# Kernel optimization log

Measured on AMD Instinct MI355X. Metric: run time of the kernel, lower is better.

The kernel has to match this reference:

```python
import jax, jax.numpy as jnp
import numpy as np

N, S, I, L, M = 4096, 8, 256, 512, 256


def setup_inputs() -> dict:
    key = jax.random.key(0)
    ks = jax.random.split(key, 13)
    sc_in = 1.0 / np.sqrt(I + L)
    sc_out = 1.0 / np.sqrt(L)
    return {
        "modulation": jax.random.normal(ks[0], (N, S * I), jnp.float32),
        "h0": jax.random.normal(ks[1], (N, S * L), jnp.float32),
        "c0": jax.random.normal(ks[2], (N, S * L), jnp.float32),
        "Wi": jax.random.normal(ks[3], (S, L, I + L), jnp.float32) * sc_in,
        "bi": jnp.full((S, L), -1.0, jnp.float32),  # init_input bias
        "Wf": jax.random.normal(ks[4], (S, L, I + L), jnp.float32) * sc_in,
        "bf": jnp.full((S, L), 1.0, jnp.float32),   # init_forget bias
        "Wg": jax.random.normal(ks[5], (S, L, I + L), jnp.float32) * sc_in,
        "bg": jnp.zeros((S, L), jnp.float32),
        "Wo": jax.random.normal(ks[6], (S, L, I + L), jnp.float32) * sc_in,
        "bo": jnp.zeros((S, L), jnp.float32),
        "Wy": jax.random.normal(ks[7], (S, M, L), jnp.float32) * sc_out,
        "by": jnp.zeros((S, M), jnp.float32),
    }


def reference(modulation, h0, c0, Wi, bi, Wf, bf, Wg, bg, Wo, bo, Wy, by):
    n = modulation.shape[0]
    x = modulation.reshape(n, S, I)          # [N,S,I]
    h = h0.reshape(n, S, L)                  # [N,S,L]
    c = c0.reshape(n, S, L)
    xh = jnp.concatenate([x, h], axis=-1)    # cat_groups: per-stream [x_s, h_s] -> [N,S,I+L]
    # grouped per-stream linear projections for the four gates
    i = jax.nn.sigmoid(jnp.einsum('nsd,sld->nsl', xh, Wi) + bi)
    f = jax.nn.sigmoid(jnp.einsum('nsd,sld->nsl', xh, Wf) + bf)
    g = jnp.tanh(jnp.einsum('nsd,sld->nsl', xh, Wg) + bg)
    o = jax.nn.sigmoid(jnp.einsum('nsd,sld->nsl', xh, Wo) + bo)
    c_new = f * c + i * g
    h_new = o * jnp.tanh(c_new)              # dropout p=0 -> identity
    y = jnp.einsum('nsl,sml->nsm', h_new, Wy) + by
    return y.reshape(n, S * M)
```

## Files before the change

### kernel.cpp

```cpp
#include <hip/hip_runtime.h>
#include <stdint.h>

#define S_ 8
#define N_ 4096
#define I_ 256
#define L_ 512
#define M_ 256
#define D_ 768

typedef __bf16 bf16x8 __attribute__((ext_vector_type(8)));
typedef float f32x4 __attribute__((ext_vector_type(4)));
typedef unsigned short ushort_t;

__device__ __forceinline__ unsigned short f2bf(float f) {
  union { float f; uint32_t u; } c; c.f = f;
  uint32_t u = c.u;
  uint32_t r = u + 0x7FFFu + ((u >> 16) & 1u);
  return (unsigned short)(r >> 16);
}

__device__ __forceinline__ float fsigmoid(float x) {
  return 1.0f / (1.0f + __expf(-x));
}
__device__ __forceinline__ float ftanh(float x) {
  float ax = fabsf(x);
  float e = __expf(-2.0f * ax);
  float t = (1.0f - e) / (1.0f + e);
  return copysignf(t, x);
}

#define GLD16(gsrc, ldst)                                                                  \
  __builtin_amdgcn_global_load_lds(                                                        \
      (const __attribute__((address_space(1))) uint32_t*)(uintptr_t)(gsrc),                \
      (__attribute__((address_space(3))) uint32_t*)(uintptr_t)(ldst), 16, 0, 0)


__global__ __launch_bounds__(256) void cast_bf16_kernel(const float* __restrict__ src,
                                                        ushort_t* __restrict__ dst, int n4) {
  int t = blockIdx.x * 256 + threadIdx.x;
  int stride = gridDim.x * 256;
  for (; t < n4; t += stride) {
    float4 v = ((const float4*)src)[t];
    ushort4 o;
    o.x = f2bf(v.x); o.y = f2bf(v.y); o.z = f2bf(v.z); o.w = f2bf(v.w);
    ((ushort4*)dst)[t] = o;
  }
}

__global__ __launch_bounds__(256) void build_xh_kernel(const float* __restrict__ mod,
                                                       const float* __restrict__ h0,
                                                       ushort_t* __restrict__ xh) {
  int t = blockIdx.x * 256 + threadIdx.x;
  const int total = S_ * N_ * (D_ / 4);
  int stride = gridDim.x * 256;
  for (; t < total; t += stride) {
    int row = t / (D_ / 4);
    int c = t - row * (D_ / 4);
    int s = row >> 12;
    int n = row & (N_ - 1);
    float4 v;
    if (c < I_ / 4)
      v = *(const float4*)(mod + (size_t)n * (S_ * I_) + s * I_ + c * 4);
    else
      v = *(const float4*)(h0 + (size_t)n * (S_ * L_) + s * L_ + (c - I_ / 4) * 4);
    ushort4 o;
    o.x = f2bf(v.x); o.y = f2bf(v.y); o.z = f2bf(v.z); o.w = f2bf(v.w);
    *(ushort4*)(xh + (size_t)t * 4) = o;
  }
}

__global__ __launch_bounds__(256, 2) void gates_kernel(
    const ushort_t* __restrict__ xh,
    const ushort_t* __restrict__ w4,
    const float* __restrict__ bi, const float* __restrict__ bff,
    const float* __restrict__ bg, const float* __restrict__ bo,
    const float* __restrict__ c0,
    ushort_t* __restrict__ hout)
{
  __shared__ __align__(16) ushort_t smem[3072 * 8];
  const int tid = threadIdx.x;
  const int lane = tid & 63;
  const int w = tid >> 6;
  const int n0 = blockIdx.x * 128;
  const int l0 = blockIdx.y * 64;
  const int s = blockIdx.z;

  f32x4 acc[4][2][4];
  #pragma unroll
  for (int g = 0; g < 4; ++g)
    #pragma unroll
    for (int rt = 0; rt < 2; ++rt)
      #pragma unroll
      for (int ct = 0; ct < 4; ++ct) {
        f32x4 z = {0.f, 0.f, 0.f, 0.f};
        acc[g][rt][ct] = z;
      }

  const size_t xh_row0 = (size_t)(s * N_ + n0) * D_;

  for (int t = 0; t < D_ / 64; ++t) {
    const int k0 = t * 64;
    #pragma unroll
    for (int it = 0; it < 4; ++it) {
      int chunk = it * 256 + tid;
      int r = chunk >> 3, c = chunk & 7;
      int cg = c ^ (r & 7);
      const ushort_t* src = xh + xh_row0 + (size_t)r * D_ + k0 + cg * 8;
      GLD16(src, &smem[(it * 256 + w * 64) * 8]);
    }
    #pragma unroll
    for (int it = 0; it < 8; ++it) {
      int chunk = it * 256 + tid;
      int g = chunk >> 9;
      int rl = (chunk >> 3) & 63;
      int c = chunk & 7;
      int cg = c ^ (rl & 7);
      const ushort_t* src = w4 + ((size_t)((g * S_ + s) * L_ + l0 + rl)) * D_ + k0 + cg * 8;
      GLD16(src, &smem[(1024 + it * 256 + w * 64) * 8]);
    }
    __syncthreads();
    #pragma unroll
    for (int kk = 0; kk < 2; ++kk) {
      const int cc = kk * 4 + (lane >> 4);
      bf16x8 a[2];
      #pragma unroll
      for (int rt = 0; rt < 2; ++rt) {
        int r = w * 32 + rt * 16 + (lane & 15);
        a[rt] = *(const bf16x8*)&smem[(r * 8 + (cc ^ (r & 7))) * 8];
      }
      #pragma unroll
      for (int g = 0; g < 4; ++g) {
        #pragma unroll
        for (int ct = 0; ct < 4; ++ct) {
          int rl = ct * 16 + (lane & 15);
          bf16x8 b = *(const bf16x8*)&smem[(1024 + (g * 64 + rl) * 8 + (cc ^ (rl & 7))) * 8];
          acc[g][0][ct] = __builtin_amdgcn_mfma_f32_16x16x32_bf16(a[0], b, acc[g][0][ct], 0, 0, 0);
          acc[g][1][ct] = __builtin_amdgcn_mfma_f32_16x16x32_bf16(a[1], b, acc[g][1][ct], 0, 0, 0);
        }
      }
    }
    __syncthreads();
  }

  #pragma unroll
  for (int ct = 0; ct < 4; ++ct) {
    const int l = l0 + ct * 16 + (lane & 15);
    const float vbi = bi[s * L_ + l];
    const float vbf = bff[s * L_ + l];
    const float vbg = bg[s * L_ + l];
    const float vbo = bo[s * L_ + l];
    #pragma unroll
    for (int rt = 0; rt < 2; ++rt) {
      #pragma unroll
      for (int j = 0; j < 4; ++j) {
        const int n = n0 + w * 32 + rt * 16 + (lane >> 4) * 4 + j;
        const float c0v = c0[(size_t)n * (S_ * L_) + s * L_ + l];
        const float iv = fsigmoid(acc[0][rt][ct][j] + vbi);
        const float fv = fsigmoid(acc[1][rt][ct][j] + vbf);
        const float gv = ftanh(acc[2][rt][ct][j] + vbg);
        const float ov = fsigmoid(acc[3][rt][ct][j] + vbo);
        const float cn = fv * c0v + iv * gv;
        const float hn = ov * ftanh(cn);
        hout[(size_t)(s * N_ + n) * L_ + l] = f2bf(hn);
      }
    }
  }
}

__global__ __launch_bounds__(256, 2) void out_kernel(
    const ushort_t* __restrict__ h,
    const ushort_t* __restrict__ wy,
    const float* __restrict__ by,
    float* __restrict__ out)
{
  __shared__ __align__(16) ushort_t smem[1536 * 8];
  const int tid = threadIdx.x;
  const int lane = tid & 63;
  const int w = tid >> 6;
  const int n0 = blockIdx.x * 128;
  const int m0 = blockIdx.y * 64;
  const int s = blockIdx.z;

  f32x4 acc[2][4];
  #pragma unroll
  for (int rt = 0; rt < 2; ++rt)
    #pragma unroll
    for (int ct = 0; ct < 4; ++ct) {
      f32x4 z = {0.f, 0.f, 0.f, 0.f};
      acc[rt][ct] = z;
    }

  const size_t h_row0 = (size_t)(s * N_ + n0) * L_;

  for (int t = 0; t < L_ / 64; ++t) {
    const int k0 = t * 64;
    #pragma unroll
    for (int it = 0; it < 4; ++it) {
      int chunk = it * 256 + tid;
      int r = chunk >> 3, c = chunk & 7;
      int cg = c ^ (r & 7);
      const ushort_t* src = h + h_row0 + (size_t)r * L_ + k0 + cg * 8;
      GLD16(src, &smem[(it * 256 + w * 64) * 8]);
    }
    #pragma unroll
    for (int it = 0; it < 2; ++it) {
      int chunk = it * 256 + tid;
      int rl = chunk >> 3, c = chunk & 7;
      int cg = c ^ (rl & 7);
      const ushort_t* src = wy + ((size_t)(s * M_ + m0 + rl)) * L_ + k0 + cg * 8;
      GLD16(src, &smem[(1024 + it * 256 + w * 64) * 8]);
    }
    __syncthreads();
    #pragma unroll
    for (int kk = 0; kk < 2; ++kk) {
      const int cc = kk * 4 + (lane >> 4);
      bf16x8 a[2];
      #pragma unroll
      for (int rt = 0; rt < 2; ++rt) {
        int r = w * 32 + rt * 16 + (lane & 15);
        a[rt] = *(const bf16x8*)&smem[(r * 8 + (cc ^ (r & 7))) * 8];
      }
      #pragma unroll
      for (int ct = 0; ct < 4; ++ct) {
        int rl = ct * 16 + (lane & 15);
        bf16x8 b = *(const bf16x8*)&smem[(1024 + rl * 8 + (cc ^ (rl & 7))) * 8];
        acc[0][ct] = __builtin_amdgcn_mfma_f32_16x16x32_bf16(a[0], b, acc[0][ct], 0, 0, 0);
        acc[1][ct] = __builtin_amdgcn_mfma_f32_16x16x32_bf16(a[1], b, acc[1][ct], 0, 0, 0);
      }
    }
    __syncthreads();
  }

  #pragma unroll
  for (int ct = 0; ct < 4; ++ct) {
    const int m = m0 + ct * 16 + (lane & 15);
    const float vb = by[s * M_ + m];
    #pragma unroll
    for (int rt = 0; rt < 2; ++rt) {
      #pragma unroll
      for (int j = 0; j < 4; ++j) {
        const int n = n0 + w * 32 + rt * 16 + (lane >> 4) * 4 + j;
        out[(size_t)n * (S_ * M_) + s * M_ + m] = acc[rt][ct][j] + vb;
      }
    }
  }
}


extern "C" void kernel_launch(void* const* d_in, const int* in_sizes, int n_in,
                              void* d_out, int out_size, void* d_ws, size_t ws_size,
                              hipStream_t stream) {
  const float* mod = (const float*)d_in[0];
  const float* h0  = (const float*)d_in[1];
  const float* c0  = (const float*)d_in[2];
  const float* Wi  = (const float*)d_in[3];
  const float* bi  = (const float*)d_in[4];
  const float* Wf  = (const float*)d_in[5];
  const float* bf  = (const float*)d_in[6];
  const float* Wg  = (const float*)d_in[7];
  const float* bg  = (const float*)d_in[8];
  const float* Wo  = (const float*)d_in[9];
  const float* bo  = (const float*)d_in[10];
  const float* Wy  = (const float*)d_in[11];
  const float* by  = (const float*)d_in[12];
  float* out = (float*)d_out;

  ushort_t* ws = (ushort_t*)d_ws;
  ushort_t* xh   = ws;
  ushort_t* w4   = xh  + (size_t)S_ * N_ * D_;
  ushort_t* wyb  = w4  + (size_t)4 * S_ * L_ * D_;
  ushort_t* hbuf = wyb + (size_t)S_ * M_ * L_;

  const int SLD4 = S_ * L_ * D_ / 4;
  cast_bf16_kernel<<<512, 256, 0, stream>>>(Wi, w4 + 0 * (size_t)S_ * L_ * D_, SLD4);
  cast_bf16_kernel<<<512, 256, 0, stream>>>(Wf, w4 + 1 * (size_t)S_ * L_ * D_, SLD4);
  cast_bf16_kernel<<<512, 256, 0, stream>>>(Wg, w4 + 2 * (size_t)S_ * L_ * D_, SLD4);
  cast_bf16_kernel<<<512, 256, 0, stream>>>(Wo, w4 + 3 * (size_t)S_ * L_ * D_, SLD4);
  cast_bf16_kernel<<<256, 256, 0, stream>>>(Wy, wyb, S_ * M_ * L_ / 4);
  build_xh_kernel<<<2048, 256, 0, stream>>>(mod, h0, xh);
  gates_kernel<<<dim3(N_ / 128, L_ / 64, S_), 256, 0, stream>>>(xh, w4, bi, bf, bg, bo, c0, hbuf);
  out_kernel<<<dim3(N_ / 128, M_ / 64, S_), 256, 0, stream>>>(hbuf, wyb, by, out);
}
```

Baseline: 227.6 us.

## Retile gates GEMM to 256x64 blocks with 512 threads, merge cast kernels

Measured after the change: 242.5 us. 1.07x slower.

```diff
diff --git a/kernel.cpp b/kernel.cpp
--- a/kernel.cpp
+++ b/kernel.cpp
@@ -7,6 +7,7 @@
 #define L_ 512
 #define M_ 256
 #define D_ 768
+#define NT32 24
 
 typedef __bf16 bf16x8 __attribute__((ext_vector_type(8)));
 typedef float f32x4 __attribute__((ext_vector_type(4)));
@@ -34,9 +35,26 @@
       (const __attribute__((address_space(1))) uint32_t*)(uintptr_t)(gsrc),                \
       (__attribute__((address_space(3))) uint32_t*)(uintptr_t)(ldst), 16, 0, 0)
 
-
-__global__ __launch_bounds__(256) void cast_bf16_kernel(const float* __restrict__ src,
-                                                        ushort_t* __restrict__ dst, int n4) {
+#define S4(rr) ((((rr) ^ ((rr) >> 2))) & 3)
+
+
+__global__ __launch_bounds__(256) void cast5_kernel(
+    const float* __restrict__ Wi, const float* __restrict__ Wf,
+    const float* __restrict__ Wg, const float* __restrict__ Wo,
+    const float* __restrict__ Wy, ushort_t* __restrict__ w4,
+    ushort_t* __restrict__ wyb) {
+  const int y = blockIdx.y;
+  const int GW = S_ * L_ * D_ / 4;
+  const float* src;
+  ushort_t* dst;
+  int n4;
+  if (y < 4) {
+    src = (y == 0) ? Wi : (y == 1) ? Wf : (y == 2) ? Wg : Wo;
+    dst = w4 + (size_t)y * S_ * L_ * D_;
+    n4 = GW;
+  } else {
+    src = Wy; dst = wyb; n4 = S_ * M_ * L_ / 4;
+  }
   int t = blockIdx.x * 256 + threadIdx.x;
   int stride = gridDim.x * 256;
   for (; t < n4; t += stride) {
@@ -50,26 +68,33 @@
 __global__ __launch_bounds__(256) void build_xh_kernel(const float* __restrict__ mod,
                                                        const float* __restrict__ h0,
                                                        ushort_t* __restrict__ xh) {
+  const int y = blockIdx.y;
   int t = blockIdx.x * 256 + threadIdx.x;
-  const int total = S_ * N_ * (D_ / 4);
   int stride = gridDim.x * 256;
-  for (; t < total; t += stride) {
-    int row = t / (D_ / 4);
-    int c = t - row * (D_ / 4);
-    int s = row >> 12;
-    int n = row & (N_ - 1);
-    float4 v;
-    if (c < I_ / 4)
-      v = *(const float4*)(mod + (size_t)n * (S_ * I_) + s * I_ + c * 4);
-    else
-      v = *(const float4*)(h0 + (size_t)n * (S_ * L_) + s * L_ + (c - I_ / 4) * 4);
-    ushort4 o;
-    o.x = f2bf(v.x); o.y = f2bf(v.y); o.z = f2bf(v.z); o.w = f2bf(v.w);
-    *(ushort4*)(xh + (size_t)t * 4) = o;
-  }
-}
-
-__global__ __launch_bounds__(256, 2) void gates_kernel(
+  if (y == 0) {
+    const int total = S_ * N_ * (I_ / 4);
+    for (; t < total; t += stride) {
+      int r = t >> 6, c = t & 63;
+      int s = r >> 12, n = r & (N_ - 1);
+      float4 v = *(const float4*)(mod + (size_t)n * (S_ * I_) + s * I_ + c * 4);
+      ushort4 o;
+      o.x = f2bf(v.x); o.y = f2bf(v.y); o.z = f2bf(v.z); o.w = f2bf(v.w);
+      *(ushort4*)(xh + (size_t)r * D_ + c * 4) = o;
+    }
+  } else {
+    const int total = S_ * N_ * (L_ / 4);
+    for (; t < total; t += stride) {
+      int r = t >> 7, c = t & 127;
+      int s = r >> 12, n = r & (N_ - 1);
+      float4 v = *(const float4*)(h0 + (size_t)n * (S_ * L_) + s * L_ + c * 4);
+      ushort4 o;
+      o.x = f2bf(v.x); o.y = f2bf(v.y); o.z = f2bf(v.z); o.w = f2bf(v.w);
+      *(ushort4*)(xh + (size_t)r * D_ + I_ + c * 4) = o;
+    }
+  }
+}
+
+__global__ __launch_bounds__(512) void gates_kernel(
     const ushort_t* __restrict__ xh,
     const ushort_t* __restrict__ w4,
     const float* __restrict__ bi, const float* __restrict__ bff,
@@ -77,88 +102,91 @@
     const float* __restrict__ c0,
     ushort_t* __restrict__ hout)
 {
-  __shared__ __align__(16) ushort_t smem[3072 * 8];
+  __shared__ __align__(16) ushort_t smem[16384];
   const int tid = threadIdx.x;
   const int lane = tid & 63;
+  const int ln15 = lane & 15;
+  const int ln4 = lane >> 4;
   const int w = tid >> 6;
-  const int n0 = blockIdx.x * 128;
-  const int l0 = blockIdx.y * 64;
-  const int s = blockIdx.z;
-
-  f32x4 acc[4][2][4];
+  const int wm = w >> 1;
+  const int wl = w & 1;
+
+  const int bid = blockIdx.x;
+  const int s = bid & 7;
+  const int r = bid >> 3;
+  const int n0 = (r >> 3) << 8;
+  const int l0 = (r & 7) << 6;
+
+  const size_t xh_base = (size_t)(s * N_ + n0) * D_;
+
+  f32x4 acc[4][8];
   #pragma unroll
-  for (int g = 0; g < 4; ++g)
-    #pragma unroll
-    for (int rt = 0; rt < 2; ++rt)
-      #pragma unroll
-      for (int ct = 0; ct < 4; ++ct) {
-        f32x4 z = {0.f, 0.f, 0.f, 0.f};
-        acc[g][rt][ct] = z;
-      }
-
-  const size_t xh_row0 = (size_t)(s * N_ + n0) * D_;
-
-  for (int t = 0; t < D_ / 64; ++t) {
-    const int k0 = t * 64;
-    #pragma unroll
-    for (int it = 0; it < 4; ++it) {
-      int chunk = it * 256 + tid;
-      int r = chunk >> 3, c = chunk & 7;
-      int cg = c ^ (r & 7);
-      const ushort_t* src = xh + xh_row0 + (size_t)r * D_ + k0 + cg * 8;
-      GLD16(src, &smem[(it * 256 + w * 64) * 8]);
-    }
-    #pragma unroll
-    for (int it = 0; it < 8; ++it) {
-      int chunk = it * 256 + tid;
-      int g = chunk >> 9;
-      int rl = (chunk >> 3) & 63;
-      int c = chunk & 7;
-      int cg = c ^ (rl & 7);
-      const ushort_t* src = w4 + ((size_t)((g * S_ + s) * L_ + l0 + rl)) * D_ + k0 + cg * 8;
-      GLD16(src, &smem[(1024 + it * 256 + w * 64) * 8]);
+  for (int i = 0; i < 4; ++i)
+    #pragma unroll
+    for (int j = 0; j < 8; ++j) {
+      f32x4 z = {0.f, 0.f, 0.f, 0.f};
+      acc[i][j] = z;
+    }
+
+  for (int t = 0; t < NT32; ++t) {
+    const int k0 = t << 5;
+    #pragma unroll
+    for (int i = 0; i < 2; ++i) {
+      int chunk = i * 512 + tid;
+      int rr = chunk >> 2, c = chunk & 3;
+      const ushort_t* src = xh + xh_base + (size_t)rr * D_ + k0 + ((c ^ S4(rr)) << 3);
+      GLD16(src, &smem[(i * 512 + (w << 6)) * 8]);
+    }
+    #pragma unroll
+    for (int i = 0; i < 2; ++i) {
+      int chunk = i * 512 + tid;
+      int rB = chunk >> 2, c = chunk & 3;
+      int g = rB >> 6, ll = rB & 63;
+      const ushort_t* src = w4 + ((size_t)((g * S_ + s) * L_) + l0 + ll) * D_ + k0 +
+                            ((c ^ S4(rB)) << 3);
+      GLD16(src, &smem[(1024 + i * 512 + (w << 6)) * 8]);
     }
     __syncthreads();
-    #pragma unroll
-    for (int kk = 0; kk < 2; ++kk) {
-      const int cc = kk * 4 + (lane >> 4);
-      bf16x8 a[2];
-      #pragma unroll
-      for (int rt = 0; rt < 2; ++rt) {
-        int r = w * 32 + rt * 16 + (lane & 15);
-        a[rt] = *(const bf16x8*)&smem[(r * 8 + (cc ^ (r & 7))) * 8];
-      }
-      #pragma unroll
-      for (int g = 0; g < 4; ++g) {
-        #pragma unroll
-        for (int ct = 0; ct < 4; ++ct) {
-          int rl = ct * 16 + (lane & 15);
-          bf16x8 b = *(const bf16x8*)&smem[(1024 + (g * 64 + rl) * 8 + (cc ^ (rl & 7))) * 8];
-          acc[g][0][ct] = __builtin_amdgcn_mfma_f32_16x16x32_bf16(a[0], b, acc[g][0][ct], 0, 0, 0);
-          acc[g][1][ct] = __builtin_amdgcn_mfma_f32_16x16x32_bf16(a[1], b, acc[g][1][ct], 0, 0, 0);
-        }
-      }
-    }
+
+    bf16x8 a[4];
+    #pragma unroll
+    for (int rt = 0; rt < 4; ++rt) {
+      int rr = (wm << 6) + (rt << 4) + ln15;
+      a[rt] = *(const bf16x8*)&smem[((rr << 2) + (ln4 ^ S4(rr))) * 8];
+    }
+    bf16x8 b[8];
+    #pragma unroll
+    for (int g = 0; g < 4; ++g)
+      #pragma unroll
+      for (int ct = 0; ct < 2; ++ct) {
+        int rB = (g << 6) + (wl << 5) + (ct << 4) + ln15;
+        b[(g << 1) + ct] = *(const bf16x8*)&smem[(1024 + (rB << 2) + (ln4 ^ S4(rB))) * 8];
+      }
+    #pragma unroll
+    for (int rt = 0; rt < 4; ++rt)
+      #pragma unroll
+      for (int cj = 0; cj < 8; ++cj)
+        acc[rt][cj] = __builtin_amdgcn_mfma_f32_16x16x32_bf16(a[rt], b[cj], acc[rt][cj], 0, 0, 0);
     __syncthreads();
   }
 
   #pragma unroll
-  for (int ct = 0; ct < 4; ++ct) {
-    const int l = l0 + ct * 16 + (lane & 15);
+  for (int ct = 0; ct < 2; ++ct) {
+    const int l = l0 + (wl << 5) + (ct << 4) + ln15;
     const float vbi = bi[s * L_ + l];
     const float vbf = bff[s * L_ + l];
     const float vbg = bg[s * L_ + l];
     const float vbo = bo[s * L_ + l];
     #pragma unroll
-    for (int rt = 0; rt < 2; ++rt) {
+    for (int rt = 0; rt < 4; ++rt) {
       #pragma unroll
       for (int j = 0; j < 4; ++j) {
-        const int n = n0 + w * 32 + rt * 16 + (lane >> 4) * 4 + j;
+        const int n = n0 + (wm << 6) + (rt << 4) + (ln4 << 2) + j;
         const float c0v = c0[(size_t)n * (S_ * L_) + s * L_ + l];
-        const float iv = fsigmoid(acc[0][rt][ct][j] + vbi);
-        const float fv = fsigmoid(acc[1][rt][ct][j] + vbf);
-        const float gv = ftanh(acc[2][rt][ct][j] + vbg);
-        const float ov = fsigmoid(acc[3][rt][ct][j] + vbo);
+        const float iv = fsigmoid(acc[rt][0 + ct][j] + vbi);
+        const float fv = fsigmoid(acc[rt][2 + ct][j] + vbf);
+        const float gv = ftanh(acc[rt][4 + ct][j] + vbg);
+        const float ov = fsigmoid(acc[rt][6 + ct][j] + vbo);
         const float cn = fv * c0v + iv * gv;
         const float hn = ov * ftanh(cn);
         hout[(size_t)(s * N_ + n) * L_ + l] = f2bf(hn);
@@ -214,18 +242,18 @@
     #pragma unroll
     for (int kk = 0; kk < 2; ++kk) {
       const int cc = kk * 4 + (lane >> 4);
-      bf16x8 a[2];
+      bf16x8 av[2];
       #pragma unroll
       for (int rt = 0; rt < 2; ++rt) {
-        int r = w * 32 + rt * 16 + (lane & 15);
-        a[rt] = *(const bf16x8*)&smem[(r * 8 + (cc ^ (r & 7))) * 8];
+        int rr = w * 32 + rt * 16 + (lane & 15);
+        av[rt] = *(const bf16x8*)&smem[(rr * 8 + (cc ^ (rr & 7))) * 8];
       }
       #pragma unroll
       for (int ct = 0; ct < 4; ++ct) {
         int rl = ct * 16 + (lane & 15);
         bf16x8 b = *(const bf16x8*)&smem[(1024 + rl * 8 + (cc ^ (rl & 7))) * 8];
-        acc[0][ct] = __builtin_amdgcn_mfma_f32_16x16x32_bf16(a[0], b, acc[0][ct], 0, 0, 0);
-        acc[1][ct] = __builtin_amdgcn_mfma_f32_16x16x32_bf16(a[1], b, acc[1][ct], 0, 0, 0);
+        acc[0][ct] = __builtin_amdgcn_mfma_f32_16x16x32_bf16(av[0], b, acc[0][ct], 0, 0, 0);
+        acc[1][ct] = __builtin_amdgcn_mfma_f32_16x16x32_bf16(av[1], b, acc[1][ct], 0, 0, 0);
       }
     }
     __syncthreads();
@@ -271,13 +299,8 @@
   ushort_t* wyb  = w4  + (size_t)4 * S_ * L_ * D_;
   ushort_t* hbuf = wyb + (size_t)S_ * M_ * L_;
 
-  const int SLD4 = S_ * L_ * D_ / 4;
-  cast_bf16_kernel<<<512, 256, 0, stream>>>(Wi, w4 + 0 * (size_t)S_ * L_ * D_, SLD4);
-  cast_bf16_kernel<<<512, 256, 0, stream>>>(Wf, w4 + 1 * (size_t)S_ * L_ * D_, SLD4);
-  cast_bf16_kernel<<<512, 256, 0, stream>>>(Wg, w4 + 2 * (size_t)S_ * L_ * D_, SLD4);
-  cast_bf16_kernel<<<512, 256, 0, stream>>>(Wo, w4 + 3 * (size_t)S_ * L_ * D_, SLD4);
-  cast_bf16_kernel<<<256, 256, 0, stream>>>(Wy, wyb, S_ * M_ * L_ / 4);
-  build_xh_kernel<<<2048, 256, 0, stream>>>(mod, h0, xh);
-  gates_kernel<<<dim3(N_ / 128, L_ / 64, S_), 256, 0, stream>>>(xh, w4, bi, bf, bg, bo, c0, hbuf);
+  cast5_kernel<<<dim3(512, 5), 256, 0, stream>>>(Wi, Wf, Wg, Wo, Wy, w4, wyb);
+  build_xh_kernel<<<dim3(2048, 2), 256, 0, stream>>>(mod, h0, xh);
+  gates_kernel<<<1024, 512, 0, stream>>>(xh, w4, bi, bf, bg, bo, c0, hbuf);
   out_kernel<<<dim3(N_ / 128, M_ / 64, S_), 256, 0, stream>>>(hbuf, wyb, by, out);
 }
```
